# Kernel optimization log

Measured on AMD Instinct MI355X. Metric: run time of the kernel, lower is better.

## Reference

```python
import jax, jax.numpy as jnp
import numpy as np

N_NODES = 100000
N_EDGES = 1600000
D_IN, D_HID, D_OUT = 128, 64, 40


def glorot(key, shape):
    lim = float(np.sqrt(6.0 / (shape[0] + shape[1])))
    return jax.random.uniform(key, shape, jnp.float32, -lim, lim)


def gcn_layer(x, W, b, src, dst, d_inv):
    # PyG GCNConv: linear first, then sym-normalized aggregation with self-loops.
    h = x @ W  # [N, d_out]
    coef = (d_inv[src] * d_inv[dst])[:, None]       # [E, 1]
    msg = h[src] * coef                              # [E, d_out] gather
    agg = jax.ops.segment_sum(msg, dst, num_segments=N_NODES)  # scatter-add
    agg = agg + h * (d_inv * d_inv)[:, None]         # self-loop contribution
    return agg + b


def setup_inputs() -> dict:
    key = jax.random.key(0)
    ks = jax.random.split(key, 8)
    x = jax.random.normal(ks[0], (N_NODES, D_IN), jnp.float32)
    edge_index = jax.random.randint(ks[1], (2, N_EDGES), 0, N_NODES, jnp.int64)
    return {
        "x": x,
        "edge_index": edge_index,
        "W1": glorot(ks[2], (D_IN, D_HID)), "b1": jnp.zeros((D_HID,), jnp.float32),
        "W2": glorot(ks[3], (D_HID, D_HID)), "b2": jnp.zeros((D_HID,), jnp.float32),
        "W3": glorot(ks[4], (D_HID, D_OUT)), "b3": jnp.zeros((D_OUT,), jnp.float32),
    }


def reference(x, edge_index, W1, b1, W2, b2, W3, b3):
    src, dst = edge_index[0], edge_index[1]
    # degree with self-loops (each node gets +1)
    deg = jax.ops.segment_sum(jnp.ones((N_EDGES,), jnp.float32), dst,
                              num_segments=N_NODES) + 1.0
    d_inv = jax.lax.rsqrt(deg)
    h = jax.nn.relu(gcn_layer(x, W1, b1, src, dst, d_inv))
    h = jax.nn.relu(gcn_layer(h, W2, b2, src, dst, d_inv))
    return gcn_layer(h, W3, b3, src, dst, d_inv)
```

## Files before the change

kernel.cpp:

```cpp
#include <hip/hip_runtime.h>
#include <hip/hip_bf16.h>


constexpr int BLK = 256;
constexpr int SB2 = 9;
constexpr int EPB = 4096;

typedef __attribute__((ext_vector_type(8))) short bf16x8;
typedef __attribute__((ext_vector_type(4))) float f32x4;

__device__ inline unsigned short bf_rne(float f) {
    unsigned int u = __float_as_uint(f);
    unsigned int r = (u + 0x7fffu + ((u >> 16) & 1u)) >> 16;
    return (unsigned short)r;
}
__device__ inline unsigned int pk(unsigned short lo, unsigned short hi) {
    return (unsigned int)lo | ((unsigned int)hi << 16);
}

__global__ __launch_bounds__(256) void part_hist(
    const int* __restrict__ dst, int* __restrict__ bh, int E, int nblk, int NB2) {
    __shared__ int lh[256];
    int k = blockIdx.x, t = threadIdx.x;
    lh[t] = 0;
    __syncthreads();
    int e0 = k * EPB;
#pragma unroll
    for (int j = 0; j < EPB / 256; ++j) {
        int e = e0 + j * 256 + t;
        if (e < E) atomicAdd(&lh[dst[e] >> SB2], 1);
    }
    __syncthreads();
    if (t < NB2) bh[t * nblk + k] = lh[t];
}

__global__ __launch_bounds__(256) void bucket_totals(
    const int* __restrict__ bh, int* __restrict__ btot, int nblk) {
    __shared__ int sh[256];
    int b = blockIdx.x, t = threadIdx.x;
    int s = 0;
    for (int i = t; i < nblk; i += 256) s += bh[b * nblk + i];
    sh[t] = s;
    __syncthreads();
    for (int off = 128; off > 0; off >>= 1) {
        if (t < off) sh[t] += sh[t + off];
        __syncthreads();
    }
    if (t == 0) btot[b] = sh[0];
}

__global__ void bucket_scan(const int* __restrict__ btot, int* __restrict__ bbase, int NB2) {
    __shared__ int sh[256];
    int t = threadIdx.x;
    int v = (t < NB2) ? btot[t] : 0;
    sh[t] = v;
    __syncthreads();
    for (int off = 1; off < 256; off <<= 1) {
        int x = (t >= off) ? sh[t - off] : 0;
        __syncthreads();
        sh[t] += x;
        __syncthreads();
    }
    if (t < NB2) bbase[t] = sh[t] - v;
}

__global__ __launch_bounds__(256) void part_scan(
    int* __restrict__ bh, const int* __restrict__ bbase, int nblk) {
    __shared__ int sh[256];
    int b = blockIdx.x, t = threadIdx.x;
    int base = bbase[b];
    int v[4]; int s = 0;
#pragma unroll
    for (int j = 0; j < 4; ++j) {
        int idx = t * 4 + j;
        v[j] = (idx < nblk) ? bh[b * nblk + idx] : 0;
        s += v[j];
    }
    sh[t] = s;
    __syncthreads();
    for (int off = 1; off < 256; off <<= 1) {
        int x = (t >= off) ? sh[t - off] : 0;
        __syncthreads();
        sh[t] += x;
        __syncthreads();
    }
    int run = sh[t] - s;
#pragma unroll
    for (int j = 0; j < 4; ++j) {
        int idx = t * 4 + j;
        if (idx < nblk) bh[b * nblk + idx] = base + run;
        run += v[j];
    }
}

__global__ __launch_bounds__(256) void part_scatter(
    const int* __restrict__ src, const int* __restrict__ dst,
    const int* __restrict__ bh, unsigned int* __restrict__ buf,
    int E, int nblk, int NB2) {
    __shared__ int lbase[256];
    __shared__ int lcnt[256];
    int k = blockIdx.x, t = threadIdx.x;
    lcnt[t] = 0;
    if (t < NB2) lbase[t] = bh[t * nblk + k];
    __syncthreads();
    int e0 = k * EPB;
#pragma unroll
    for (int j = 0; j < EPB / 256; ++j) {
        int e = e0 + j * 256 + t;
        if (e < E) {
            int d = dst[e];
            int b = d >> SB2;
            int p = lbase[b] + atomicAdd(&lcnt[b], 1);
            buf[p] = ((unsigned int)(d & ((1 << SB2) - 1)) << 23) | (unsigned int)src[e];
        }
    }
}

__global__ __launch_bounds__(256) void csr_finalize(
    const unsigned int* __restrict__ buf, const int* __restrict__ bbase,
    int* __restrict__ row_ptr, float* __restrict__ dinv,
    int* __restrict__ csr, int N, int E, int NB2) {
    __shared__ int hist[1 << SB2];
    __shared__ int excl[1 << SB2];
    __shared__ int ssc[256];
    int b = blockIdx.x, t = threadIdx.x;
    int nb0 = b << SB2;
    int nn = N - nb0; if (nn > (1 << SB2)) nn = 1 << SB2;
    int beg = bbase[b];
    int end = (b + 1 < NB2) ? bbase[b + 1] : E;

    hist[t] = 0; hist[t + 256] = 0;
    __syncthreads();
    for (int i = beg + t; i < end; i += 256)
        atomicAdd(&hist[buf[i] >> 23], 1);
    __syncthreads();

    int a0 = hist[2 * t], a1 = hist[2 * t + 1];
    int s = a0 + a1;
    ssc[t] = s;
    __syncthreads();
    for (int off = 1; off < 256; off <<= 1) {
        int x = (t >= off) ? ssc[t - off] : 0;
        __syncthreads();
        ssc[t] += x;
        __syncthreads();
    }
    int run = ssc[t] - s;
    excl[2 * t] = run;
    excl[2 * t + 1] = run + a0;
    __syncthreads();

    for (int j = t; j < nn; j += 256) {
        row_ptr[nb0 + j] = beg + excl[j];
        dinv[nb0 + j] = rsqrtf((float)hist[j] + 1.0f);
    }
    if (b == NB2 - 1 && t == 0) row_ptr[N] = E;
    __syncthreads();

    hist[t] = 0; hist[t + 256] = 0;
    __syncthreads();
    for (int i = beg + t; i < end; i += 256) {
        unsigned int w = buf[i];
        int local = w >> 23;
        int p = beg + excl[local] + atomicAdd(&hist[local], 1);
        csr[p] = (int)(w & 0x7fffffu);
    }
}

template<int K, int NOUT, bool AFP32>
__global__ __launch_bounds__(256) void gemm_mfma(
    const void* __restrict__ Aptr, const float* __restrict__ W,
    const float* __restrict__ d_inv, unsigned short* __restrict__ hs, int M)
{
    __shared__ unsigned short Wt[64][K + 8];
    __shared__ float Cst[64][68];

    const int t = threadIdx.x;
    const int wave = t >> 6, lane = t & 63;
    const int m = lane & 15, kq = lane >> 4;

    for (int idx = t; idx < K * 64; idx += 256) {
        int k = idx >> 6, c = idx & 63;
        float wv = (c < NOUT) ? W[k * NOUT + c] : 0.0f;
        Wt[c][k] = bf_rne(wv);
    }
    __syncthreads();

    const int rb = blockIdx.x * 64;
    int arow = rb + wave * 16 + m;
    if (arow >= M) arow = M - 1;

    f32x4 acc[4] = {{0.f,0.f,0.f,0.f},{0.f,0.f,0.f,0.f},
                    {0.f,0.f,0.f,0.f},{0.f,0.f,0.f,0.f}};
    union Frag { bf16x8 v; unsigned short u[8]; };

#pragma unroll
    for (int kc = 0; kc < K / 32; ++kc) {
        const int kbase = kc * 32 + kq * 8;
        Frag a;
        if (AFP32) {
            const float* ap = (const float*)Aptr + (size_t)arow * K + kbase;
            float4 x0 = *(const float4*)ap;
            float4 x1 = *(const float4*)(ap + 4);
            a.u[0] = bf_rne(x0.x); a.u[1] = bf_rne(x0.y);
            a.u[2] = bf_rne(x0.z); a.u[3] = bf_rne(x0.w);
            a.u[4] = bf_rne(x1.x); a.u[5] = bf_rne(x1.y);
            a.u[6] = bf_rne(x1.z); a.u[7] = bf_rne(x1.w);
        } else {
            const unsigned short* ap = (const unsigned short*)Aptr + (size_t)arow * 64 + kbase;
            a.v = *(const bf16x8*)ap;
        }
#pragma unroll
        for (int ct = 0; ct < 4; ++ct) {
            Frag b;
            b.v = *(const bf16x8*)(&Wt[ct * 16 + m][kbase]);
            acc[ct] = __builtin_amdgcn_mfma_f32_16x16x32_bf16(a.v, b.v, acc[ct], 0, 0, 0);
        }
    }

#pragma unroll
    for (int ct = 0; ct < 4; ++ct)
#pragma unroll
        for (int r = 0; r < 4; ++r)
            Cst[wave * 16 + kq * 4 + r][ct * 16 + m] = acc[ct][r];
    __syncthreads();

    int row = t >> 2, seg = t & 3;
    int grow = rb + row;
    if (grow < M) {
        float di = d_inv[grow];
        unsigned int uu[8];
#pragma unroll
        for (int j = 0; j < 8; ++j) {
            float v0 = Cst[row][seg * 16 + 2 * j]     * di;
            float v1 = Cst[row][seg * 16 + 2 * j + 1] * di;
            uu[j] = pk(bf_rne(v0), bf_rne(v1));
        }
        unsigned short* orow = hs + (size_t)grow * 64 + seg * 16;
        *(uint4*)orow       = make_uint4(uu[0], uu[1], uu[2], uu[3]);
        *((uint4*)orow + 1) = make_uint4(uu[4], uu[5], uu[6], uu[7]);
    }
}

template<int DACT, bool RELU, bool OBF16, int OSTRIDE>
__global__ __launch_bounds__(256) void agg8(
    const unsigned short* __restrict__ hs, const int* __restrict__ row_ptr,
    const int* __restrict__ csr, const float* __restrict__ dinv,
    const float* __restrict__ b, void* __restrict__ out, int N)
{
    int wave = (blockIdx.x * 256 + threadIdx.x) >> 6;
    int lane = threadIdx.x & 63;
    if (wave >= N) return;
    int i = wave;
    int g = lane >> 3, q = lane & 7;
    const uint4* hsv = (const uint4*)hs;

    int beg = row_ptr[i], end = row_ptr[i + 1];
    float acc[8] = {0.f, 0.f, 0.f, 0.f, 0.f, 0.f, 0.f, 0.f};

    for (int c = beg; c < end; c += 64) {
        int m = end - c; if (m > 64) m = 64;
        int s_l = (c + lane < end) ? csr[c + lane] : 0;
        int nIter = (m + 7) >> 3;
        for (int k = 0; k < nIter; ++k) {
            int ei = k * 8 + g;
            int s = __shfl(s_l, ei, 64);
            if (ei < m) {
                uint4 u = hsv[(size_t)s * 8 + q];
                acc[0] += __uint_as_float(u.x << 16);
                acc[1] += __uint_as_float(u.x & 0xffff0000u);
                acc[2] += __uint_as_float(u.y << 16);
                acc[3] += __uint_as_float(u.y & 0xffff0000u);
                acc[4] += __uint_as_float(u.z << 16);
                acc[5] += __uint_as_float(u.z & 0xffff0000u);
                acc[6] += __uint_as_float(u.w << 16);
                acc[7] += __uint_as_float(u.w & 0xffff0000u);
            }
        }
    }

#pragma unroll
    for (int off = 8; off < 64; off <<= 1)
#pragma unroll
        for (int j = 0; j < 8; ++j)
            acc[j] += __shfl_xor(acc[j], off, 64);

    if (g == 0 && q * 8 < DACT) {
        uint4 u = hsv[(size_t)i * 8 + q];
        acc[0] += __uint_as_float(u.x << 16);
        acc[1] += __uint_as_float(u.x & 0xffff0000u);
        acc[2] += __uint_as_float(u.y << 16);
        acc[3] += __uint_as_float(u.y & 0xffff0000u);
        acc[4] += __uint_as_float(u.z << 16);
        acc[5] += __uint_as_float(u.z & 0xffff0000u);
        acc[6] += __uint_as_float(u.w << 16);
        acc[7] += __uint_as_float(u.w & 0xffff0000u);
        float di = dinv[i];
#pragma unroll
        for (int j = 0; j < 8; ++j) {
            acc[j] = di * acc[j] + b[q * 8 + j];
            if (RELU) acc[j] = fmaxf(acc[j], 0.0f);
        }
        if (OBF16) {
            unsigned short* ob = (unsigned short*)out;
            uint4 o;
            o.x = pk(bf_rne(acc[0]), bf_rne(acc[1]));
            o.y = pk(bf_rne(acc[2]), bf_rne(acc[3]));
            o.z = pk(bf_rne(acc[4]), bf_rne(acc[5]));
            o.w = pk(bf_rne(acc[6]), bf_rne(acc[7]));
            *(uint4*)(ob + (size_t)i * 64 + q * 8) = o;
        } else {
            float* of = (float*)out;
            *(float4*)(of + (size_t)i * OSTRIDE + q * 8) =
                make_float4(acc[0], acc[1], acc[2], acc[3]);
            *(float4*)(of + (size_t)i * OSTRIDE + q * 8 + 4) =
                make_float4(acc[4], acc[5], acc[6], acc[7]);
        }
    }
}

extern "C" void kernel_launch(void* const* d_in, const int* in_sizes, int n_in,
                              void* d_out, int out_size, void* d_ws, size_t ws_size,
                              hipStream_t stream) {
    const float* x   = (const float*)d_in[0];
    const int*   ei  = (const int*)  d_in[1];
    const float* W1  = (const float*)d_in[2];
    const float* bb1 = (const float*)d_in[3];
    const float* W2  = (const float*)d_in[4];
    const float* bb2 = (const float*)d_in[5];
    const float* W3  = (const float*)d_in[6];
    const float* bb3 = (const float*)d_in[7];
    float* out = (float*)d_out;

    const int N = in_sizes[0] / 128;
    const int E = in_sizes[1] / 2;
    const int* src = ei;
    const int* dst = ei + E;
    const int NB2  = (N + (1 << SB2) - 1) >> SB2;
    const int nblk = (E + EPB - 1) / EPB;

    float* ws = (float*)d_ws;
    const size_t NP  = ((size_t)N + 255) & ~255ull;
    float* dinv = ws;
    unsigned short* bufHs  = (unsigned short*)(ws + NP);
    unsigned short* bufAct = bufHs + (size_t)N * 64;
    int*   row_ptr = (int*)(bufAct + (size_t)N * 64);
    int*   btot    = row_ptr + (((size_t)N + 2) & ~1ull);
    int*   bbase   = btot + 256;
    int*   bh      = bbase + 256;
    size_t bhsz    = ((size_t)NB2 * nblk + 1) & ~1ull;
    unsigned int* buf = (unsigned int*)(bh + bhsz);
    int*   csr     = (int*)(buf + E);

    dim3 blk(BLK);
    int gRows = (N + 63) / 64;
    int gWave = (N * 64 + BLK - 1) / BLK;

    part_hist<<<nblk, blk, 0, stream>>>(dst, bh, E, nblk, NB2);
    bucket_totals<<<NB2, blk, 0, stream>>>(bh, btot, nblk);
    bucket_scan<<<1, blk, 0, stream>>>(btot, bbase, NB2);
    part_scan<<<NB2, blk, 0, stream>>>(bh, bbase, nblk);
    part_scatter<<<nblk, blk, 0, stream>>>(src, dst, bh, buf, E, nblk, NB2);
    csr_finalize<<<NB2, blk, 0, stream>>>(buf, bbase, row_ptr, dinv, csr, N, E, NB2);

    gemm_mfma<128, 64, true><<<gRows, blk, 0, stream>>>(x, W1, dinv, bufHs, N);
    agg8<64, true, true, 64><<<gWave, blk, 0, stream>>>(bufHs, row_ptr, csr, dinv, bb1, bufAct, N);

    gemm_mfma<64, 64, false><<<gRows, blk, 0, stream>>>(bufAct, W2, dinv, bufHs, N);
    agg8<64, true, true, 64><<<gWave, blk, 0, stream>>>(bufHs, row_ptr, csr, dinv, bb2, bufAct, N);

    gemm_mfma<64, 40, false><<<gRows, blk, 0, stream>>>(bufAct, W3, dinv, bufHs, N);
    agg8<40, false, false, 40><<<gWave, blk, 0, stream>>>(bufHs, row_ptr, csr, dinv, bb3, out, N);
}
```

Before: 325.9 us.

## Aggregate each node with a 16-lane quarter-wave instead of a full wave

The aggregation kernel now assigns one node to 16 lanes, each lane owning 4 bf16 features and walking all neighbors serially, instead of one node per 64-lane wave that splits neighbors over 8 groups and reduces them with cross-lane shuffles. This removes the shuffle-xor reduction, the idle lanes in the epilogue and most of the padding waste for the average degree of about 16. The cost is more loop iterations per lane, a longer dependent accumulation chain, and divergence between quarter-waves whose nodes have different degrees.

```diff
diff --git a/kernel.cpp b/kernel.cpp
--- a/kernel.cpp
+++ b/kernel.cpp
@@ -243,78 +243,56 @@
 }
 
 template<int DACT, bool RELU, bool OBF16, int OSTRIDE>
-__global__ __launch_bounds__(256) void agg8(
+__global__ __launch_bounds__(256) void agg4(
     const unsigned short* __restrict__ hs, const int* __restrict__ row_ptr,
     const int* __restrict__ csr, const float* __restrict__ dinv,
     const float* __restrict__ b, void* __restrict__ out, int N)
 {
-    int wave = (blockIdx.x * 256 + threadIdx.x) >> 6;
+    int i = (blockIdx.x * 256 + threadIdx.x) >> 4;
+    if (i >= N) return;
     int lane = threadIdx.x & 63;
-    if (wave >= N) return;
-    int i = wave;
-    int g = lane >> 3, q = lane & 7;
-    const uint4* hsv = (const uint4*)hs;
+    int q  = lane & 15;
+    int sb = lane & 48;
 
     int beg = row_ptr[i], end = row_ptr[i + 1];
-    float acc[8] = {0.f, 0.f, 0.f, 0.f, 0.f, 0.f, 0.f, 0.f};
-
-    for (int c = beg; c < end; c += 64) {
-        int m = end - c; if (m > 64) m = 64;
-        int s_l = (c + lane < end) ? csr[c + lane] : 0;
-        int nIter = (m + 7) >> 3;
-        for (int k = 0; k < nIter; ++k) {
-            int ei = k * 8 + g;
-            int s = __shfl(s_l, ei, 64);
-            if (ei < m) {
-                uint4 u = hsv[(size_t)s * 8 + q];
-                acc[0] += __uint_as_float(u.x << 16);
-                acc[1] += __uint_as_float(u.x & 0xffff0000u);
-                acc[2] += __uint_as_float(u.y << 16);
-                acc[3] += __uint_as_float(u.y & 0xffff0000u);
-                acc[4] += __uint_as_float(u.z << 16);
-                acc[5] += __uint_as_float(u.z & 0xffff0000u);
-                acc[6] += __uint_as_float(u.w << 16);
-                acc[7] += __uint_as_float(u.w & 0xffff0000u);
-            }
-        }
-    }
-
-#pragma unroll
-    for (int off = 8; off < 64; off <<= 1)
-#pragma unroll
-        for (int j = 0; j < 8; ++j)
-            acc[j] += __shfl_xor(acc[j], off, 64);
-
-    if (g == 0 && q * 8 < DACT) {
-        uint4 u = hsv[(size_t)i * 8 + q];
-        acc[0] += __uint_as_float(u.x << 16);
-        acc[1] += __uint_as_float(u.x & 0xffff0000u);
-        acc[2] += __uint_as_float(u.y << 16);
-        acc[3] += __uint_as_float(u.y & 0xffff0000u);
-        acc[4] += __uint_as_float(u.z << 16);
-        acc[5] += __uint_as_float(u.z & 0xffff0000u);
-        acc[6] += __uint_as_float(u.w << 16);
-        acc[7] += __uint_as_float(u.w & 0xffff0000u);
+
+    uint2 u0 = *(const uint2*)(hs + (size_t)i * 64 + q * 4);
+    float a0 = __uint_as_float(u0.x << 16);
+    float a1 = __uint_as_float(u0.x & 0xffff0000u);
+    float a2 = __uint_as_float(u0.y << 16);
+    float a3 = __uint_as_float(u0.y & 0xffff0000u);
+
+    for (int c = beg; c < end; c += 16) {
+        int s_l = (c + q < end) ? csr[c + q] : 0;
+        int m = end - c; if (m > 16) m = 16;
+        for (int k = 0; k < m; ++k) {
+            int s = __shfl(s_l, sb | k, 64);
+            uint2 u = *(const uint2*)(hs + (size_t)s * 64 + q * 4);
+            a0 += __uint_as_float(u.x << 16);
+            a1 += __uint_as_float(u.x & 0xffff0000u);
+            a2 += __uint_as_float(u.y << 16);
+            a3 += __uint_as_float(u.y & 0xffff0000u);
+        }
+    }
+
+    if (q * 4 < DACT) {
         float di = dinv[i];
-#pragma unroll
-        for (int j = 0; j < 8; ++j) {
-            acc[j] = di * acc[j] + b[q * 8 + j];
-            if (RELU) acc[j] = fmaxf(acc[j], 0.0f);
+        const float4 bv = *(const float4*)(b + q * 4);
+        a0 = di * a0 + bv.x; a1 = di * a1 + bv.y;
+        a2 = di * a2 + bv.z; a3 = di * a3 + bv.w;
+        if (RELU) {
+            a0 = fmaxf(a0, 0.f); a1 = fmaxf(a1, 0.f);
+            a2 = fmaxf(a2, 0.f); a3 = fmaxf(a3, 0.f);
         }
         if (OBF16) {
             unsigned short* ob = (unsigned short*)out;
-            uint4 o;
-            o.x = pk(bf_rne(acc[0]), bf_rne(acc[1]));
-            o.y = pk(bf_rne(acc[2]), bf_rne(acc[3]));
-            o.z = pk(bf_rne(acc[4]), bf_rne(acc[5]));
-            o.w = pk(bf_rne(acc[6]), bf_rne(acc[7]));
-            *(uint4*)(ob + (size_t)i * 64 + q * 8) = o;
+            uint2 o;
+            o.x = pk(bf_rne(a0), bf_rne(a1));
+            o.y = pk(bf_rne(a2), bf_rne(a3));
+            *(uint2*)(ob + (size_t)i * 64 + q * 4) = o;
         } else {
             float* of = (float*)out;
-            *(float4*)(of + (size_t)i * OSTRIDE + q * 8) =
-                make_float4(acc[0], acc[1], acc[2], acc[3]);
-            *(float4*)(of + (size_t)i * OSTRIDE + q * 8 + 4) =
-                make_float4(acc[4], acc[5], acc[6], acc[7]);
+            *(float4*)(of + (size_t)i * OSTRIDE + q * 4) = make_float4(a0, a1, a2, a3);
         }
     }
 }
@@ -354,7 +332,7 @@
 
     dim3 blk(BLK);
     int gRows = (N + 63) / 64;
-    int gWave = (N * 64 + BLK - 1) / BLK;
+    int gQW   = (N * 16 + BLK - 1) / BLK;
 
     part_hist<<<nblk, blk, 0, stream>>>(dst, bh, E, nblk, NB2);
     bucket_totals<<<NB2, blk, 0, stream>>>(bh, btot, nblk);
@@ -364,11 +342,11 @@
     csr_finalize<<<NB2, blk, 0, stream>>>(buf, bbase, row_ptr, dinv, csr, N, E, NB2);
 
     gemm_mfma<128, 64, true><<<gRows, blk, 0, stream>>>(x, W1, dinv, bufHs, N);
-    agg8<64, true, true, 64><<<gWave, blk, 0, stream>>>(bufHs, row_ptr, csr, dinv, bb1, bufAct, N);
+    agg4<64, true, true, 64><<<gQW, blk, 0, stream>>>(bufHs, row_ptr, csr, dinv, bb1, bufAct, N);
 
     gemm_mfma<64, 64, false><<<gRows, blk, 0, stream>>>(bufAct, W2, dinv, bufHs, N);
-    agg8<64, true, true, 64><<<gWave, blk, 0, stream>>>(bufHs, row_ptr, csr, dinv, bb2, bufAct, N);
+    agg4<64, true, true, 64><<<gQW, blk, 0, stream>>>(bufHs, row_ptr, csr, dinv, bb2, bufAct, N);
 
     gemm_mfma<64, 40, false><<<gRows, blk, 0, stream>>>(bufAct, W3, dinv, bufHs, N);
-    agg8<40, false, false, 40><<<gWave, blk, 0, stream>>>(bufHs, row_ptr, csr, dinv, bb3, out, N);
-}
+    agg4<40, false, false, 40><<<gQW, blk, 0, stream>>>(bufHs, row_ptr, csr, dinv, bb3, out, N);
+}
```

New measurement: 319.1 us. 2.1% less time.
